# Kernel tuning notes

Measured on AMD Instinct MI355X. Metric: run time of the kernel, lower is better.

## Reference

```python
import jax, jax.numpy as jnp
import numpy as np

N_NODES = 100000
N_EDGES = 1600000
IN_FEATS = 256
OUT_FEATS = 128


def setup_inputs() -> dict:
    key = jax.random.key(0)
    k1, k2, k3, k4, k5, k6 = jax.random.split(key, 6)
    feat = jax.random.normal(k1, (N_NODES, IN_FEATS), dtype=jnp.float32)
    # xavier_uniform-style scale for the weight
    limit = float(np.sqrt(6.0 / (IN_FEATS + OUT_FEATS)))
    weight = jax.random.uniform(k2, (IN_FEATS, OUT_FEATS), dtype=jnp.float32, minval=-limit, maxval=limit)
    # degree-normalizer scalars per node (positive, like 1/sqrt(deg))
    cj = jax.random.uniform(k3, (N_NODES, 1), dtype=jnp.float32, minval=0.05, maxval=1.0)
    ci = jax.random.uniform(k4, (N_NODES, 1), dtype=jnp.float32, minval=0.05, maxval=1.0)
    src = jax.random.randint(k5, (N_EDGES,), 0, N_NODES, dtype=jnp.int32)
    dst = jax.random.randint(k6, (N_EDGES,), 0, N_NODES, dtype=jnp.int32)
    return {"feat": feat, "weight": weight, "cj": cj, "ci": ci, "src": src, "dst": dst}


def reference(feat, weight, cj, ci, src, dst):
    # dense transform: [N, in] @ [in, out] -> [N, out]
    h = feat @ weight
    # pre-scale by source normalizer (dropout rate 0 -> identity)
    h = h * cj
    # copy_src + sum aggregation: gather messages at src, scatter-sum into dst
    msgs = h[src]  # [E, out]
    agg = jax.ops.segment_sum(msgs, dst, num_segments=N_NODES)  # [N, out]
    # post-scale by destination normalizer
    return agg * ci
```

## Files before the change

kernel.cpp:

```cpp
#include <hip/hip_runtime.h>

#define N_NODES 100000
#define N_EDGES 1600000
#define IN_F 256
#define OUT_F 128
#define E4 (N_EDGES / 4)

#define BUCKETS 256
#define NPB 391
#define CH 4096
#define NCHUNK ((N_EDGES + CH - 1) / CH)
#define CAP 8192

#define GEMM_BLOCKS ((N_NODES + 127) / 128)
#define GP_BLOCKS (GEMM_BLOCKS + NCHUNK)

typedef short bf16x8 __attribute__((ext_vector_type(8)));
typedef float f32x4 __attribute__((ext_vector_type(4)));

__device__ __forceinline__ unsigned int f2bf(float f) {
    unsigned int u = __float_as_uint(f);
    return (u + 0x7FFFu + ((u >> 16) & 1u)) >> 16;
}
__device__ __forceinline__ unsigned int pack2(float a, float b) {
    return f2bf(a) | (f2bf(b) << 16);
}
__device__ __forceinline__ float bf_lo(unsigned int u) { return __uint_as_float(u << 16); }
__device__ __forceinline__ float bf_hi(unsigned int u) { return __uint_as_float(u & 0xFFFF0000u); }

__global__ __launch_bounds__(256) void wprep_kernel(const float* __restrict__ W,
                                                    unsigned short* __restrict__ Wfrag) {
    int idx = blockIdx.x * 256 + threadIdx.x;
    if (idx < IN_F * OUT_F) {
        int j    = idx & 7;
        int lane = (idx >> 3) & 63;
        int fkt  = idx >> 9;
        int f    = fkt >> 3;
        int kt   = fkt & 7;
        int c    = f * 16 + (lane & 15);
        int k    = kt * 32 + (lane >> 4) * 8 + j;
        Wfrag[idx] = (unsigned short)f2bf(W[k * OUT_F + c]);
    }
}

__global__ __launch_bounds__(512) void gemm_part_kernel(const float* __restrict__ feat,
                                                        const unsigned short* __restrict__ Wfrag,
                                                        const float* __restrict__ cj,
                                                        unsigned short* __restrict__ h,
                                                        const int* __restrict__ src,
                                                        const int* __restrict__ dst,
                                                        int* __restrict__ bucket_cursor,
                                                        uint2* __restrict__ slab) {
    __shared__ __align__(16) char pool[65536];

    const int bid = blockIdx.x;
    const int tid = threadIdx.x;

    if (bid >= GEMM_BLOCKS) {
        int* hist   = (int*)pool;
        int* hstart = hist + 256;
        int* gbase  = hstart + 256;
        uint2* stage = (uint2*)(pool + 3072);

        const int cb = bid - GEMM_BLOCKS;
        const int e0 = cb * CH;
        int nE = N_EDGES - e0;
        if (nE > CH) nE = CH;

        if (tid < 256) hist[tid] = 0;
        __syncthreads();

        int dv[8], rk[8];
        const int4* d4 = reinterpret_cast<const int4*>(dst);
        #pragma unroll
        for (int i = 0; i < 2; ++i) {
            int li = tid + i * 512;
            int g4 = (e0 >> 2) + li;
            if (li * 4 < nE && g4 < E4) {
                int4 d = d4[g4];
                dv[i*4+0] = d.x; dv[i*4+1] = d.y; dv[i*4+2] = d.z; dv[i*4+3] = d.w;
                rk[i*4+0] = atomicAdd(&hist[d.x / NPB], 1);
                rk[i*4+1] = atomicAdd(&hist[d.y / NPB], 1);
                rk[i*4+2] = atomicAdd(&hist[d.z / NPB], 1);
                rk[i*4+3] = atomicAdd(&hist[d.w / NPB], 1);
            } else {
                dv[i*4+0] = -1; dv[i*4+1] = -1; dv[i*4+2] = -1; dv[i*4+3] = -1;
            }
        }
        __syncthreads();

        int v = 0;
        if (tid < 256) { v = hist[tid]; hstart[tid] = v; }
        __syncthreads();
        #pragma unroll
        for (int off = 1; off < 256; off <<= 1) {
            int u = 0;
            if (tid < 256 && tid >= off) u = hstart[tid - off];
            __syncthreads();
            if (tid < 256) hstart[tid] += u;
            __syncthreads();
        }
        if (tid < 256) {
            int ex = hstart[tid] - v;
            if (v > 0) gbase[tid] = atomicAdd(&bucket_cursor[tid], v);
            hstart[tid] = ex;
        }
        __syncthreads();

        const int4* s4 = reinterpret_cast<const int4*>(src);
        #pragma unroll
        for (int i = 0; i < 2; ++i) {
            int li = tid + i * 512;
            int g4 = (e0 >> 2) + li;
            if (dv[i*4] >= 0) {
                int4 s = s4[g4];
                stage[hstart[dv[i*4+0] / NPB] + rk[i*4+0]] = make_uint2((unsigned)dv[i*4+0], (unsigned)s.x);
                stage[hstart[dv[i*4+1] / NPB] + rk[i*4+1]] = make_uint2((unsigned)dv[i*4+1], (unsigned)s.y);
                stage[hstart[dv[i*4+2] / NPB] + rk[i*4+2]] = make_uint2((unsigned)dv[i*4+2], (unsigned)s.z);
                stage[hstart[dv[i*4+3] / NPB] + rk[i*4+3]] = make_uint2((unsigned)dv[i*4+3], (unsigned)s.w);
            }
        }
        __syncthreads();

        for (int idx = tid; idx < nE; idx += 512) {
            uint2 p = stage[idx];
            int b = (int)p.x / NPB;
            slab[(size_t)b * CAP + gbase[b] + (idx - hstart[b])] = p;
        }
        return;
    }

    unsigned short* wl = (unsigned short*)pool;

    const int wave = tid >> 6;
    const int lane = tid & 63;
    const int r  = lane & 15;
    const int kq = lane >> 4;
    const int rowbase = bid * 128 + wave * 16;

    int arow = rowbase + r;
    if (arow >= N_NODES) arow = N_NODES - 1;
    const float4* fr4 = reinterpret_cast<const float4*>(feat + (size_t)arow * IN_F);

    float4 fv[16];
    #pragma unroll
    for (int kt = 0; kt < 8; ++kt) {
        fv[2 * kt]     = fr4[kt * 8 + kq * 2];
        fv[2 * kt + 1] = fr4[kt * 8 + kq * 2 + 1];
    }

    {
        const uint4* wsrc = reinterpret_cast<const uint4*>(Wfrag);
        uint4* wdst = reinterpret_cast<uint4*>(wl);
        #pragma unroll
        for (int i = 0; i < 8; ++i) wdst[tid + i * 512] = wsrc[tid + i * 512];
    }

    bf16x8 a[8];
    #pragma unroll
    for (int kt = 0; kt < 8; ++kt) {
        uint4 au;
        au.x = pack2(fv[2 * kt].x,     fv[2 * kt].y);
        au.y = pack2(fv[2 * kt].z,     fv[2 * kt].w);
        au.z = pack2(fv[2 * kt + 1].x, fv[2 * kt + 1].y);
        au.w = pack2(fv[2 * kt + 1].z, fv[2 * kt + 1].w);
        a[kt] = *reinterpret_cast<bf16x8*>(&au);
    }
    __syncthreads();

    f32x4 acc[8];
    #pragma unroll
    for (int f = 0; f < 8; ++f) acc[f] = (f32x4){0.f, 0.f, 0.f, 0.f};

    #pragma unroll
    for (int kt = 0; kt < 8; ++kt) {
        #pragma unroll
        for (int f = 0; f < 8; ++f) {
            bf16x8 b = *reinterpret_cast<const bf16x8*>(&wl[((f * 8 + kt) * 64 + lane) * 8]);
            acc[f] = __builtin_amdgcn_mfma_f32_16x16x32_bf16(a[kt], b, acc[f], 0, 0, 0);
        }
    }

    int orow[4]; float cjv[4];
    #pragma unroll
    for (int i = 0; i < 4; ++i) {
        orow[i] = rowbase + kq * 4 + i;
        cjv[i] = cj[orow[i] < N_NODES ? orow[i] : 0];
    }

    __syncthreads();
    unsigned short* wout = (unsigned short*)pool + wave * (16 * 136);
    #pragma unroll
    for (int f = 0; f < 8; ++f) {
        #pragma unroll
        for (int i = 0; i < 4; ++i) {
            wout[(kq * 4 + i) * 136 + f * 16 + r] =
                (unsigned short)f2bf(acc[f][i] * cjv[i]);
        }
    }
    __syncthreads();

    {
        int row = lane >> 2;
        int ch  = lane & 3;
        int grow = rowbase + row;
        if (grow < N_NODES) {
            uint4* hv = reinterpret_cast<uint4*>(h);
            #pragma unroll
            for (int j = 0; j < 4; ++j) {
                uint4 vv = *reinterpret_cast<const uint4*>(
                    (const char*)wout + row * 272 + (ch + 4 * j) * 16);
                hv[(size_t)grow * 16 + ch + 4 * j] = vv;
            }
        }
    }
}

__global__ __launch_bounds__(256) void scan256_kernel(const int* __restrict__ bucket_cursor,
                                                      int* __restrict__ bucket_gbase,
                                                      int* __restrict__ offsets) {
    __shared__ int s[256];
    int t = threadIdx.x;
    int v = bucket_cursor[t];
    s[t] = v;
    __syncthreads();
    #pragma unroll
    for (int off = 1; off < 256; off <<= 1) {
        int u = (t >= off) ? s[t - off] : 0;
        __syncthreads();
        s[t] += u;
        __syncthreads();
    }
    bucket_gbase[t] = s[t] - v;
    if (t == 0) offsets[N_NODES] = N_EDGES;
}

__global__ __launch_bounds__(256) void bin_kernel(const uint2* __restrict__ slab,
                                                  const int* __restrict__ bucket_cursor,
                                                  const int* __restrict__ bucket_gbase,
                                                  int* __restrict__ offsets,
                                                  int* __restrict__ bin_src) {
    __shared__ int hist[392];
    __shared__ int cur[392];
    __shared__ int sbuf[256];

    const int b = blockIdx.x;
    const int t = threadIdx.x;
    const int nlo = b * NPB;
    int nn = N_NODES - nlo;
    if (nn > NPB) nn = NPB;
    const int sz = bucket_cursor[b];
    const int gb = bucket_gbase[b];
    const uint2* sl = slab + (size_t)b * CAP;

    for (int j = t; j < 392; j += 256) hist[j] = 0;
    __syncthreads();

    for (int i = t; i < sz; i += 256) atomicAdd(&hist[(int)sl[i].x - nlo], 1);
    __syncthreads();

    int a0 = 0, a1 = 0;
    if (t < 196) { a0 = hist[2 * t]; a1 = hist[2 * t + 1]; }
    int part = a0 + a1;
    sbuf[t] = part;
    __syncthreads();
    #pragma unroll
    for (int off = 1; off < 256; off <<= 1) {
        int u = (t >= off) ? sbuf[t - off] : 0;
        __syncthreads();
        sbuf[t] += u;
        __syncthreads();
    }
    int ex = sbuf[t] - part;
    if (t < 196) {
        int o0 = gb + ex;
        int o1 = o0 + a0;
        if (2 * t < nn)     { offsets[nlo + 2 * t]     = o0; cur[2 * t]     = o0; }
        if (2 * t + 1 < nn) { offsets[nlo + 2 * t + 1] = o1; cur[2 * t + 1] = o1; }
    }
    __syncthreads();

    for (int i = t; i < sz; i += 256) {
        uint2 p = sl[i];
        int pos = atomicAdd(&cur[(int)p.x - nlo], 1);
        bin_src[pos] = (int)p.y;
    }
}

__global__ __launch_bounds__(256) void gather_kernel(const uint4* __restrict__ h4,
                                                     const float* __restrict__ ci,
                                                     const int* __restrict__ offsets,
                                                     const int* __restrict__ bin_src,
                                                     float* __restrict__ out) {
    int node = blockIdx.x * 16 + (threadIdx.x >> 4);
    int lane = threadIdx.x & 15;
    if (node >= N_NODES) return;

    int beg = offsets[node];
    int end = offsets[node + 1];

    float acc[8] = {};
    int i = beg;
    for (; i + 4 <= end; i += 4) {
        int s0 = bin_src[i + 0];
        int s1 = bin_src[i + 1];
        int s2 = bin_src[i + 2];
        int s3 = bin_src[i + 3];
        uint4 v0 = h4[(size_t)s0 * 16 + lane];
        uint4 v1 = h4[(size_t)s1 * 16 + lane];
        uint4 v2 = h4[(size_t)s2 * 16 + lane];
        uint4 v3 = h4[(size_t)s3 * 16 + lane];
        acc[0] += (bf_lo(v0.x) + bf_lo(v1.x)) + (bf_lo(v2.x) + bf_lo(v3.x));
        acc[1] += (bf_hi(v0.x) + bf_hi(v1.x)) + (bf_hi(v2.x) + bf_hi(v3.x));
        acc[2] += (bf_lo(v0.y) + bf_lo(v1.y)) + (bf_lo(v2.y) + bf_lo(v3.y));
        acc[3] += (bf_hi(v0.y) + bf_hi(v1.y)) + (bf_hi(v2.y) + bf_hi(v3.y));
        acc[4] += (bf_lo(v0.z) + bf_lo(v1.z)) + (bf_lo(v2.z) + bf_lo(v3.z));
        acc[5] += (bf_hi(v0.z) + bf_hi(v1.z)) + (bf_hi(v2.z) + bf_hi(v3.z));
        acc[6] += (bf_lo(v0.w) + bf_lo(v1.w)) + (bf_lo(v2.w) + bf_lo(v3.w));
        acc[7] += (bf_hi(v0.w) + bf_hi(v1.w)) + (bf_hi(v2.w) + bf_hi(v3.w));
    }
    for (; i < end; ++i) {
        int s = bin_src[i];
        uint4 v = h4[(size_t)s * 16 + lane];
        acc[0] += bf_lo(v.x); acc[1] += bf_hi(v.x);
        acc[2] += bf_lo(v.y); acc[3] += bf_hi(v.y);
        acc[4] += bf_lo(v.z); acc[5] += bf_hi(v.z);
        acc[6] += bf_lo(v.w); acc[7] += bf_hi(v.w);
    }
    float sc = ci[node];
    float4 o0 = make_float4(acc[0] * sc, acc[1] * sc, acc[2] * sc, acc[3] * sc);
    float4 o1 = make_float4(acc[4] * sc, acc[5] * sc, acc[6] * sc, acc[7] * sc);
    float4* o4 = reinterpret_cast<float4*>(out) + (size_t)node * 32 + lane * 2;
    o4[0] = o0;
    o4[1] = o1;
}

extern "C" void kernel_launch(void* const* d_in, const int* in_sizes, int n_in,
                              void* d_out, int out_size, void* d_ws, size_t ws_size,
                              hipStream_t stream) {
    const float* feat = (const float*)d_in[0];
    const float* W    = (const float*)d_in[1];
    const float* cj   = (const float*)d_in[2];
    const float* ci   = (const float*)d_in[3];
    const int*   src  = (const int*)d_in[4];
    const int*   dst  = (const int*)d_in[5];
    float* out = (float*)d_out;

    const size_t H_BYTES   = (size_t)N_NODES * OUT_F * 2;
    const size_t WT_BYTES  = (size_t)IN_F * OUT_F * 2;
    const size_t OFF_BYTES = (((size_t)(N_NODES + 1) * 4) + 15) & ~(size_t)15;
    const size_t BC_BYTES  = (size_t)BUCKETS * 4;
    const size_t BG_BYTES  = (((size_t)BUCKETS * 4) + 15) & ~(size_t)15;
    const size_t SLAB_BYTES = (size_t)BUCKETS * CAP * 8;

    char* ws = (char*)d_ws;
    unsigned short* h     = (unsigned short*)ws;  ws += H_BYTES;
    unsigned short* Wfrag = (unsigned short*)ws;  ws += WT_BYTES;
    int* offsets        = (int*)ws;   ws += OFF_BYTES;
    int* bucket_cursor  = (int*)ws;   ws += BC_BYTES;
    int* bucket_gbase   = (int*)ws;   ws += BG_BYTES;
    uint2* slab         = (uint2*)ws; ws += SLAB_BYTES;
    int* bin_src        = (int*)ws;

    wprep_kernel<<<128, 256, 0, stream>>>(W, Wfrag);
    hipMemsetAsync(bucket_cursor, 0, BC_BYTES, stream);

    gemm_part_kernel<<<GP_BLOCKS, 512, 0, stream>>>(feat, Wfrag, cj, h, src, dst,
                                                    bucket_cursor, slab);

    scan256_kernel<<<1, 256, 0, stream>>>(bucket_cursor, bucket_gbase, offsets);
    bin_kernel<<<BUCKETS, 256, 0, stream>>>(slab, bucket_cursor, bucket_gbase, offsets, bin_src);

    gather_kernel<<<(N_NODES + 15) / 16, 256, 0, stream>>>((const uint4*)h, ci, offsets, bin_src, out);
}
```

Measured before the change: 126.4 us.

## Persistent GEMM tiles with prefetch, fold memset and scan into neighbor kernels

GEMM blocks now each process four 128-row tiles, loading W fragments into LDS once per block and prefetching the next tile's feature rows while the MFMAs for the current tile run. The bucket-cursor memset moves into the weight-prep kernel, and the single-block scan kernel is removed; every bin block recomputes the 256-entry prefix scan itself. This cuts two launches and repeated W loads, at the cost of fewer GEMM blocks (less parallelism), a larger LDS footprint per block, and redundant scan work in each bin block.

```diff
diff --git a/kernel.cpp b/kernel.cpp
--- a/kernel.cpp
+++ b/kernel.cpp
@@ -12,7 +12,8 @@
 #define NCHUNK ((N_EDGES + CH - 1) / CH)
 #define CAP 8192
 
-#define GEMM_BLOCKS ((N_NODES + 127) / 128)
+#define GEMM_T 4
+#define GEMM_BLOCKS 196
 #define GP_BLOCKS (GEMM_BLOCKS + NCHUNK)
 
 typedef short bf16x8 __attribute__((ext_vector_type(8)));
@@ -28,8 +29,9 @@
 __device__ __forceinline__ float bf_lo(unsigned int u) { return __uint_as_float(u << 16); }
 __device__ __forceinline__ float bf_hi(unsigned int u) { return __uint_as_float(u & 0xFFFF0000u); }
 
-__global__ __launch_bounds__(256) void wprep_kernel(const float* __restrict__ W,
-                                                    unsigned short* __restrict__ Wfrag) {
+__global__ __launch_bounds__(256) void setup_kernel(const float* __restrict__ W,
+                                                    unsigned short* __restrict__ Wfrag,
+                                                    int* __restrict__ bucket_cursor) {
     int idx = blockIdx.x * 256 + threadIdx.x;
     if (idx < IN_F * OUT_F) {
         int j    = idx & 7;
@@ -41,6 +43,7 @@
         int k    = kt * 32 + (lane >> 4) * 8 + j;
         Wfrag[idx] = (unsigned short)f2bf(W[k * OUT_F + c]);
     }
+    if (blockIdx.x == 0 && threadIdx.x < BUCKETS) bucket_cursor[threadIdx.x] = 0;
 }
 
 __global__ __launch_bounds__(512) void gemm_part_kernel(const float* __restrict__ feat,
@@ -51,7 +54,7 @@
                                                         const int* __restrict__ dst,
                                                         int* __restrict__ bucket_cursor,
                                                         uint2* __restrict__ slab) {
-    __shared__ __align__(16) char pool[65536];
+    __shared__ __align__(16) char pool[65536 + 8 * 16 * 136 * 2];
 
     const int bid = blockIdx.x;
     const int tid = threadIdx.x;
@@ -131,22 +134,22 @@
     }
 
     unsigned short* wl = (unsigned short*)pool;
-
     const int wave = tid >> 6;
     const int lane = tid & 63;
     const int r  = lane & 15;
     const int kq = lane >> 4;
-    const int rowbase = bid * 128 + wave * 16;
-
-    int arow = rowbase + r;
-    if (arow >= N_NODES) arow = N_NODES - 1;
-    const float4* fr4 = reinterpret_cast<const float4*>(feat + (size_t)arow * IN_F);
+    unsigned short* wout = (unsigned short*)(pool + 65536) + wave * (16 * 136);
 
     float4 fv[16];
-    #pragma unroll
-    for (int kt = 0; kt < 8; ++kt) {
-        fv[2 * kt]     = fr4[kt * 8 + kq * 2];
-        fv[2 * kt + 1] = fr4[kt * 8 + kq * 2 + 1];
+    {
+        int arow = bid * 512 + wave * 16 + r;
+        if (arow >= N_NODES) arow = N_NODES - 1;
+        const float4* fr4 = reinterpret_cast<const float4*>(feat + (size_t)arow * IN_F);
+        #pragma unroll
+        for (int kt = 0; kt < 8; ++kt) {
+            fv[2 * kt]     = fr4[kt * 8 + kq * 2];
+            fv[2 * kt + 1] = fr4[kt * 8 + kq * 2 + 1];
+        }
     }
 
     {
@@ -155,102 +158,111 @@
         #pragma unroll
         for (int i = 0; i < 8; ++i) wdst[tid + i * 512] = wsrc[tid + i * 512];
     }
-
-    bf16x8 a[8];
-    #pragma unroll
-    for (int kt = 0; kt < 8; ++kt) {
-        uint4 au;
-        au.x = pack2(fv[2 * kt].x,     fv[2 * kt].y);
-        au.y = pack2(fv[2 * kt].z,     fv[2 * kt].w);
-        au.z = pack2(fv[2 * kt + 1].x, fv[2 * kt + 1].y);
-        au.w = pack2(fv[2 * kt + 1].z, fv[2 * kt + 1].w);
-        a[kt] = *reinterpret_cast<bf16x8*>(&au);
-    }
-    __syncthreads();
-
-    f32x4 acc[8];
-    #pragma unroll
-    for (int f = 0; f < 8; ++f) acc[f] = (f32x4){0.f, 0.f, 0.f, 0.f};
-
-    #pragma unroll
-    for (int kt = 0; kt < 8; ++kt) {
+    __syncthreads();
+
+    for (int t = 0; t < GEMM_T; ++t) {
+        const int rowbase = bid * 512 + t * 128 + wave * 16;
+
+        bf16x8 a[8];
+        #pragma unroll
+        for (int kt = 0; kt < 8; ++kt) {
+            uint4 au;
+            au.x = pack2(fv[2 * kt].x,     fv[2 * kt].y);
+            au.y = pack2(fv[2 * kt].z,     fv[2 * kt].w);
+            au.z = pack2(fv[2 * kt + 1].x, fv[2 * kt + 1].y);
+            au.w = pack2(fv[2 * kt + 1].z, fv[2 * kt + 1].w);
+            a[kt] = *reinterpret_cast<bf16x8*>(&au);
+        }
+
+        if (t < GEMM_T - 1) {
+            int arow = bid * 512 + (t + 1) * 128 + wave * 16 + r;
+            if (arow >= N_NODES) arow = N_NODES - 1;
+            const float4* fr4 = reinterpret_cast<const float4*>(feat + (size_t)arow * IN_F);
+            #pragma unroll
+            for (int kt = 0; kt < 8; ++kt) {
+                fv[2 * kt]     = fr4[kt * 8 + kq * 2];
+                fv[2 * kt + 1] = fr4[kt * 8 + kq * 2 + 1];
+            }
+        }
+
+        f32x4 acc[8];
+        #pragma unroll
+        for (int f = 0; f < 8; ++f) acc[f] = (f32x4){0.f, 0.f, 0.f, 0.f};
+
+        #pragma unroll
+        for (int kt = 0; kt < 8; ++kt) {
+            #pragma unroll
+            for (int f = 0; f < 8; ++f) {
+                bf16x8 b = *reinterpret_cast<const bf16x8*>(&wl[((f * 8 + kt) * 64 + lane) * 8]);
+                acc[f] = __builtin_amdgcn_mfma_f32_16x16x32_bf16(a[kt], b, acc[f], 0, 0, 0);
+            }
+        }
+
+        int orow[4]; float cjv[4];
+        #pragma unroll
+        for (int i = 0; i < 4; ++i) {
+            orow[i] = rowbase + kq * 4 + i;
+            cjv[i] = cj[orow[i] < N_NODES ? orow[i] : 0];
+        }
+
         #pragma unroll
         for (int f = 0; f < 8; ++f) {
-            bf16x8 b = *reinterpret_cast<const bf16x8*>(&wl[((f * 8 + kt) * 64 + lane) * 8]);
-            acc[f] = __builtin_amdgcn_mfma_f32_16x16x32_bf16(a[kt], b, acc[f], 0, 0, 0);
-        }
-    }
-
-    int orow[4]; float cjv[4];
-    #pragma unroll
-    for (int i = 0; i < 4; ++i) {
-        orow[i] = rowbase + kq * 4 + i;
-        cjv[i] = cj[orow[i] < N_NODES ? orow[i] : 0];
-    }
-
-    __syncthreads();
-    unsigned short* wout = (unsigned short*)pool + wave * (16 * 136);
-    #pragma unroll
-    for (int f = 0; f < 8; ++f) {
-        #pragma unroll
-        for (int i = 0; i < 4; ++i) {
-            wout[(kq * 4 + i) * 136 + f * 16 + r] =
-                (unsigned short)f2bf(acc[f][i] * cjv[i]);
-        }
-    }
-    __syncthreads();
-
-    {
-        int row = lane >> 2;
-        int ch  = lane & 3;
-        int grow = rowbase + row;
-        if (grow < N_NODES) {
-            uint4* hv = reinterpret_cast<uint4*>(h);
             #pragma unroll
-            for (int j = 0; j < 4; ++j) {
-                uint4 vv = *reinterpret_cast<const uint4*>(
-                    (const char*)wout + row * 272 + (ch + 4 * j) * 16);
-                hv[(size_t)grow * 16 + ch + 4 * j] = vv;
-            }
-        }
-    }
-}
-
-__global__ __launch_bounds__(256) void scan256_kernel(const int* __restrict__ bucket_cursor,
-                                                      int* __restrict__ bucket_gbase,
-                                                      int* __restrict__ offsets) {
-    __shared__ int s[256];
-    int t = threadIdx.x;
-    int v = bucket_cursor[t];
-    s[t] = v;
-    __syncthreads();
-    #pragma unroll
-    for (int off = 1; off < 256; off <<= 1) {
-        int u = (t >= off) ? s[t - off] : 0;
-        __syncthreads();
-        s[t] += u;
-        __syncthreads();
-    }
-    bucket_gbase[t] = s[t] - v;
-    if (t == 0) offsets[N_NODES] = N_EDGES;
+            for (int i = 0; i < 4; ++i) {
+                wout[(kq * 4 + i) * 136 + f * 16 + r] =
+                    (unsigned short)f2bf(acc[f][i] * cjv[i]);
+            }
+        }
+        __syncthreads();
+
+        {
+            int row = lane >> 2;
+            int ch  = lane & 3;
+            int grow = rowbase + row;
+            if (grow < N_NODES) {
+                uint4* hv = reinterpret_cast<uint4*>(h);
+                #pragma unroll
+                for (int j = 0; j < 4; ++j) {
+                    uint4 vv = *reinterpret_cast<const uint4*>(
+                        (const char*)wout + row * 272 + (ch + 4 * j) * 16);
+                    hv[(size_t)grow * 16 + ch + 4 * j] = vv;
+                }
+            }
+        }
+        __syncthreads();
+    }
 }
 
 __global__ __launch_bounds__(256) void bin_kernel(const uint2* __restrict__ slab,
                                                   const int* __restrict__ bucket_cursor,
-                                                  const int* __restrict__ bucket_gbase,
                                                   int* __restrict__ offsets,
                                                   int* __restrict__ bin_src) {
     __shared__ int hist[392];
     __shared__ int cur[392];
     __shared__ int sbuf[256];
+    __shared__ int gb_sh, sz_sh;
 
     const int b = blockIdx.x;
     const int t = threadIdx.x;
     const int nlo = b * NPB;
     int nn = N_NODES - nlo;
     if (nn > NPB) nn = NPB;
-    const int sz = bucket_cursor[b];
-    const int gb = bucket_gbase[b];
+
+    int v = bucket_cursor[t];
+    sbuf[t] = v;
+    __syncthreads();
+    #pragma unroll
+    for (int off = 1; off < 256; off <<= 1) {
+        int u = (t >= off) ? sbuf[t - off] : 0;
+        __syncthreads();
+        sbuf[t] += u;
+        __syncthreads();
+    }
+    if (t == b) { gb_sh = sbuf[t] - v; sz_sh = v; }
+    if (b == 0 && t == 0) offsets[N_NODES] = N_EDGES;
+    __syncthreads();
+    const int gb = gb_sh;
+    const int sz = sz_sh;
     const uint2* sl = slab + (size_t)b * CAP;
 
     for (int j = t; j < 392; j += 256) hist[j] = 0;
@@ -349,8 +361,7 @@
     const size_t H_BYTES   = (size_t)N_NODES * OUT_F * 2;
     const size_t WT_BYTES  = (size_t)IN_F * OUT_F * 2;
     const size_t OFF_BYTES = (((size_t)(N_NODES + 1) * 4) + 15) & ~(size_t)15;
-    const size_t BC_BYTES  = (size_t)BUCKETS * 4;
-    const size_t BG_BYTES  = (((size_t)BUCKETS * 4) + 15) & ~(size_t)15;
+    const size_t BC_BYTES  = (((size_t)BUCKETS * 4) + 15) & ~(size_t)15;
     const size_t SLAB_BYTES = (size_t)BUCKETS * CAP * 8;
 
     char* ws = (char*)d_ws;
@@ -358,18 +369,15 @@
     unsigned short* Wfrag = (unsigned short*)ws;  ws += WT_BYTES;
     int* offsets        = (int*)ws;   ws += OFF_BYTES;
     int* bucket_cursor  = (int*)ws;   ws += BC_BYTES;
-    int* bucket_gbase   = (int*)ws;   ws += BG_BYTES;
     uint2* slab         = (uint2*)ws; ws += SLAB_BYTES;
     int* bin_src        = (int*)ws;
 
-    wprep_kernel<<<128, 256, 0, stream>>>(W, Wfrag);
-    hipMemsetAsync(bucket_cursor, 0, BC_BYTES, stream);
+    setup_kernel<<<128, 256, 0, stream>>>(W, Wfrag, bucket_cursor);
 
     gemm_part_kernel<<<GP_BLOCKS, 512, 0, stream>>>(feat, Wfrag, cj, h, src, dst,
                                                     bucket_cursor, slab);
 
-    scan256_kernel<<<1, 256, 0, stream>>>(bucket_cursor, bucket_gbase, offsets);
-    bin_kernel<<<BUCKETS, 256, 0, stream>>>(slab, bucket_cursor, bucket_gbase, offsets, bin_src);
+    bin_kernel<<<BUCKETS, 256, 0, stream>>>(slab, bucket_cursor, offsets, bin_src);
 
     gather_kernel<<<(N_NODES + 15) / 16, 256, 0, stream>>>((const uint4*)h, ci, offsets, bin_src, out);
 }
```

Measured after the change: 124.8 us. No clear change (-1.2%).
